# Kernel tuning notes

Hardware: AMD Instinct MI355X
Metric: run time of the kernel (lower is better)

The kernel has to match this reference:

```python
import jax, jax.numpy as jnp
import numpy as np
from jax import lax

NODATA_VALUE = 0.0
RADIUS = 16  # structuring element size = 2*RADIUS + 1 = 33


def setup_inputs() -> dict:
    key = jax.random.key(0)
    # binary-ish raster: ~half pixels equal the nodata value (0.0)
    x = jax.random.randint(key, (8, 2048, 2048, 1), 0, 2).astype(jnp.float32)
    return {"x": x}


def reference(x):
    # nodata mask: 1 where x == nodata, else 0 (uint8 in original; float here for reduce_window)
    mask = jnp.where(jnp.equal(x, NODATA_VALUE), 1.0, 0.0).astype(x.dtype)
    se = 1 + 2 * RADIUS
    # tf.nn.dilation2d with an all-zeros kernel == sliding-window max over (se x se),
    # SAME padding. A square max window is separable: row-max then column-max.
    m = lax.reduce_window(mask, -jnp.inf, lax.max,
                          window_dimensions=(1, se, 1, 1),
                          window_strides=(1, 1, 1, 1),
                          padding="SAME")
    m = lax.reduce_window(m, -jnp.inf, lax.max,
                          window_dimensions=(1, 1, se, 1),
                          window_strides=(1, 1, 1, 1),
                          padding="SAME")
    return m.astype(jnp.uint8)
```

## Files before the change

kernel.cpp:

```cpp
#include <hip/hip_runtime.h>
#include <stdint.h>


#define HH_ 2048
#define WW_PX 2048
#define WW 32
#define RAD 16
#define ROWS 8
#define SR (ROWS + 2 * RAD)
#define TPB2 256

typedef int vint4 __attribute__((ext_vector_type(4)));

__global__ __launch_bounds__(256) void pack_kernel(const float* __restrict__ x,
                                                   uint64_t* __restrict__ packed) {
  const int t = threadIdx.x;
  const int lane = t & 63;
  const int wv = t >> 6;
  const float* rp = x + (long long)blockIdx.x * WW_PX + (wv << 9) + lane;
  uint64_t* pr = packed + (long long)blockIdx.x * WW + (wv << 3);

  float v[8];
#pragma unroll
  for (int j = 0; j < 8; ++j)
    v[j] = __builtin_nontemporal_load(rp + (j << 6));
#pragma unroll
  for (int j = 0; j < 8; ++j) {
    const unsigned long long b = __ballot(v[j] == 0.0f);
    if (lane == j) pr[j] = b;
  }
}

__global__ __launch_bounds__(TPB2) void dilate_kernel(const uint64_t* __restrict__ packed,
                                                      int* __restrict__ out) {
  __shared__ uint64_t stage[SR][WW];

  const int t = threadIdx.x;
  const int gr0 = blockIdx.x * ROWS;
  const int n = gr0 >> 11;
  const int h0 = gr0 & 2047;
  const uint64_t* base = packed + (long long)n * (HH_ * WW);

#pragma unroll
  for (int i = 0; i < SR * WW / TPB2; ++i) {
    const int idx = i * TPB2 + t;
    const int rr = idx >> 5;
    const int w_ = idx & 31;
    int hh = h0 + rr - RAD;
    hh = hh < 0 ? 0 : (hh > HH_ - 1 ? HH_ - 1 : hh);
    stage[rr][w_] = base[hh * WW + w_];
  }
  __syncthreads();

  const int lane = t & 63;
  const int wv = t >> 6;
  const int w = lane & 31;
  const int h = lane >> 5;
  const int r = wv * 2 + h;

  uint64_t v = 0;
#pragma unroll
  for (int i = 0; i <= 2 * RAD; ++i) v |= stage[r + i][w];

  const uint64_t p  = (w == 0)  ? 0ull : __shfl(v, lane - 1);
  const uint64_t nx = (w == 31) ? 0ull : __shfl(v, lane + 1);
  uint64_t res = v;
#pragma unroll
  for (int s = 1; s <= RAD; ++s) {
    res |= (v >> s) | (nx << (64 - s));
    res |= (v << s) | (p >> (64 - s));
  }

  int* optr = out + (long long)(gr0 + wv * 2) * WW_PX;
#pragma unroll
  for (int it = 0; it < 16; ++it) {
    const int f = it * 64 + lane;
    const int row_l = f >> 9;
    const int wi = (f >> 4) & 31;
    const int sh = (f & 15) * 4;
    const uint64_t bits = __shfl(res, row_l * 32 + wi) >> sh;
    vint4 o;
    o.x = (int)(bits & 1);
    o.y = (int)((bits >> 1) & 1);
    o.z = (int)((bits >> 2) & 1);
    o.w = (int)((bits >> 3) & 1);
    __builtin_nontemporal_store(o, (vint4*)(optr + (long long)f * 4));
  }
}

extern "C" void kernel_launch(void* const* d_in, const int* in_sizes, int n_in,
                              void* d_out, int out_size, void* d_ws, size_t ws_size,
                              hipStream_t stream) {
  const float* x = (const float*)d_in[0];
  int* out = (int*)d_out;
  uint64_t* packed = (uint64_t*)d_ws;

  hipLaunchKernelGGL(pack_kernel, dim3(16384), dim3(256), 0, stream, x, packed);
  hipLaunchKernelGGL(dilate_kernel, dim3(2048), dim3(TPB2), 0, stream, packed, out);
}
```

Before: 223.6 us.

## Fuse pack and dilate into one kernel with per-block flag handoff

```diff
diff --git a/kernel.cpp b/kernel.cpp
--- a/kernel.cpp
+++ b/kernel.cpp
@@ -2,62 +2,92 @@
 #include <stdint.h>
 
 
-#define HH_ 2048
-#define WW_PX 2048
+#define HH 2048
+#define WPX 2048
 #define WW 32
 #define RAD 16
 #define ROWS 8
 #define SR (ROWS + 2 * RAD)
-#define TPB2 256
+#define TPB 256
+#define NBLK 2048
 
 typedef int vint4 __attribute__((ext_vector_type(4)));
 
-__global__ __launch_bounds__(256) void pack_kernel(const float* __restrict__ x,
-                                                   uint64_t* __restrict__ packed) {
+__global__ __launch_bounds__(256) void init_flags(unsigned* __restrict__ flags) {
+  flags[blockIdx.x * 256 + threadIdx.x] = 0u;
+}
+
+__global__ __launch_bounds__(TPB, 8) void pc_kernel(const float* __restrict__ x,
+                                                    uint64_t* __restrict__ packed,
+                                                    unsigned* __restrict__ flags,
+                                                    int* __restrict__ out) {
+  __shared__ uint64_t stage[SR][WW];
+
+  const int bid = blockIdx.x;
+  const int b = ((bid & 7) << 8) | (bid >> 3);
   const int t = threadIdx.x;
   const int lane = t & 63;
   const int wv = t >> 6;
-  const float* rp = x + (long long)blockIdx.x * WW_PX + (wv << 9) + lane;
-  uint64_t* pr = packed + (long long)blockIdx.x * WW + (wv << 3);
 
-  float v[8];
+  const int gr0 = b * ROWS;
+  const int n = gr0 >> 11;
+  const int h0 = gr0 & (HH - 1);
+
+  {
+    const float* xr = x + (long long)gr0 * WPX;
+    uint64_t* prow = packed + (long long)gr0 * WW;
 #pragma unroll
-  for (int j = 0; j < 8; ++j)
-    v[j] = __builtin_nontemporal_load(rp + (j << 6));
+    for (int rr = 0; rr < 2; ++rr) {
+      const int row = (wv << 1) + rr;
+      const float* rp = xr + (long long)row * WPX + lane;
+      uint64_t* pw = prow + row * WW;
 #pragma unroll
-  for (int j = 0; j < 8; ++j) {
-    const unsigned long long b = __ballot(v[j] == 0.0f);
-    if (lane == j) pr[j] = b;
+      for (int bch = 0; bch < 4; ++bch) {
+        float v[8];
+#pragma unroll
+        for (int j = 0; j < 8; ++j)
+          v[j] = __builtin_nontemporal_load(rp + (((bch << 3) + j) << 6));
+#pragma unroll
+        for (int j = 0; j < 8; ++j) {
+          const unsigned long long m = __ballot(v[j] == 0.0f);
+          if (lane == j) pw[(bch << 3) + j] = m;
+        }
+      }
+    }
   }
-}
+  __threadfence();
+  __syncthreads();
+  if (t == 0)
+    __hip_atomic_store(&flags[b], 1u, __ATOMIC_RELEASE, __HIP_MEMORY_SCOPE_AGENT);
 
-__global__ __launch_bounds__(TPB2) void dilate_kernel(const uint64_t* __restrict__ packed,
-                                                      int* __restrict__ out) {
-  __shared__ uint64_t stage[SR][WW];
-
-  const int t = threadIdx.x;
-  const int gr0 = blockIdx.x * ROWS;
-  const int n = gr0 >> 11;
-  const int h0 = gr0 & 2047;
-  const uint64_t* base = packed + (long long)n * (HH_ * WW);
-
-#pragma unroll
-  for (int i = 0; i < SR * WW / TPB2; ++i) {
-    const int idx = i * TPB2 + t;
-    const int rr = idx >> 5;
-    const int w_ = idx & 31;
-    int hh = h0 + rr - RAD;
-    hh = hh < 0 ? 0 : (hh > HH_ - 1 ? HH_ - 1 : hh);
-    stage[rr][w_] = base[hh * WW + w_];
+  const int img_b0 = n << 8;
+  const int img_b1 = img_b0 + 255;
+  if (t < 5) {
+    int nb = b - 2 + t;
+    nb = nb < img_b0 ? img_b0 : (nb > img_b1 ? img_b1 : nb);
+    while (__hip_atomic_load(&flags[nb], __ATOMIC_ACQUIRE,
+                             __HIP_MEMORY_SCOPE_AGENT) == 0u)
+      __builtin_amdgcn_s_sleep(4);
   }
   __syncthreads();
 
-  const int lane = t & 63;
-  const int wv = t >> 6;
+  {
+    const uint64_t* base = packed + (((long long)n << 11) * WW);
+#pragma unroll
+    for (int i = 0; i < SR * WW / TPB; ++i) {
+      const int idx = i * TPB + t;
+      const int rr = idx >> 5;
+      const int w_ = idx & 31;
+      int hh = h0 + rr - RAD;
+      hh = hh < 0 ? 0 : (hh > HH - 1 ? HH - 1 : hh);
+      stage[rr][w_] = base[hh * WW + w_];
+    }
+  }
+  __syncthreads();
+
   const int w = lane & 31;
   const int h = lane >> 5;
-  const int r = wv * 2 + h;
-
+  const int r = (wv << 1) + h;
   uint64_t v = 0;
 #pragma unroll
   for (int i = 0; i <= 2 * RAD; ++i) v |= stage[r + i][w];
@@ -71,14 +101,14 @@
     res |= (v << s) | (p >> (64 - s));
   }
 
-  int* optr = out + (long long)(gr0 + wv * 2) * WW_PX;
+  int* optr = out + (long long)(gr0 + (wv << 1)) * WPX;
 #pragma unroll
   for (int it = 0; it < 16; ++it) {
-    const int f = it * 64 + lane;
+    const int f = (it << 6) + lane;
     const int row_l = f >> 9;
     const int wi = (f >> 4) & 31;
-    const int sh = (f & 15) * 4;
-    const uint64_t bits = __shfl(res, row_l * 32 + wi) >> sh;
+    const int sh = (f & 15) << 2;
+    const uint64_t bits = __shfl(res, (row_l << 5) + wi) >> sh;
     vint4 o;
     o.x = (int)(bits & 1);
     o.y = (int)((bits >> 1) & 1);
@@ -94,7 +124,9 @@
   const float* x = (const float*)d_in[0];
   int* out = (int*)d_out;
   uint64_t* packed = (uint64_t*)d_ws;
+  unsigned* flags = (unsigned*)((char*)d_ws + (4u << 20));
 
-  hipLaunchKernelGGL(pack_kernel, dim3(16384), dim3(256), 0, stream, x, packed);
-  hipLaunchKernelGGL(dilate_kernel, dim3(2048), dim3(TPB2), 0, stream, packed, out);
+  hipLaunchKernelGGL(init_flags, dim3(8), dim3(256), 0, stream, flags);
+  hipLaunchKernelGGL(pc_kernel, dim3(NBLK), dim3(TPB), 0, stream,
+                     x, packed, flags, out);
 }
```

Measured after the change: 581.0 us. 2.6x slower.
